# Performance work log

Measured on AMD Instinct MI355X. Metric: run time of the kernel, lower is better.

## Reference

```python
import jax, jax.numpy as jnp
import numpy as np

N = 50000      # nodes
E = 400000     # edges per relation
R = 3          # edge types
D = 128        # input_dim == hidden_dim
H = 8          # attention heads
Dh = D // H    # per-head dim (16)
OUT = 1        # output logits
NEG_SLOPE = 0.2
LN_EPS = 1e-5


def setup_inputs() -> dict:
    key = jax.random.key(0)
    ks = jax.random.split(key, 20)
    s = 0.05
    f32 = jnp.float32
    return {
        "feat": jax.random.normal(ks[0], (N, D), f32),
        "edge_src": jax.random.randint(ks[1], (R, E), 0, N, dtype=jnp.int32),
        "edge_dst": jax.random.randint(ks[2], (R, E), 0, N, dtype=jnp.int32),
        # conv1: per-relation GATConv params (W, attn_l, attn_r, bias)
        "W1": jax.random.normal(ks[3], (R, D, H * Dh), f32) * s,
        "al1": jax.random.normal(ks[4], (R, H, Dh), f32) * s,
        "ar1": jax.random.normal(ks[5], (R, H, Dh), f32) * s,
        "b1": jnp.zeros((R, H * Dh), f32),
        # conv2
        "W2": jax.random.normal(ks[6], (R, D, H * Dh), f32) * s,
        "al2": jax.random.normal(ks[7], (R, H, Dh), f32) * s,
        "ar2": jax.random.normal(ks[8], (R, H, Dh), f32) * s,
        "b2": jnp.zeros((R, H * Dh), f32),
        # LayerNorm
        "ln_g": jnp.ones((D,), f32),
        "ln_b": jnp.zeros((D,), f32),
        # classifier MLP (dropout inactive at eval)
        "Wc1": jax.random.normal(ks[9], (D, D), f32) * s,
        "bc1": jnp.zeros((D,), f32),
        "Wc2": jax.random.normal(ks[10], (D, OUT), f32) * s,
        "bc2": jnp.zeros((OUT,), f32),
    }


def _gat(x, src, dst, W, al, ar, b):
    """DGL GATConv on one relation: x [N,Din] -> [N, H*Dh]."""
    h = (x @ W).reshape(N, H, Dh)                       # projected feats
    el = (h * al).sum(-1)                               # [N,H] src attn term
    er = (h * ar).sum(-1)                               # [N,H] dst attn term
    e = jax.nn.leaky_relu(el[src] + er[dst], NEG_SLOPE)  # [E,H]
    # edge-softmax over incoming edges per dst node, per head
    m = jax.ops.segment_max(e, dst, num_segments=N)     # [N,H]
    ex = jnp.exp(e - m[dst])
    denom = jax.ops.segment_sum(ex, dst, num_segments=N)
    alpha = ex / denom[dst]                             # [E,H]
    msg = alpha[:, :, None] * h[src]                    # [E,H,Dh]
    out = jax.ops.segment_sum(msg, dst, num_segments=N)  # [N,H,Dh]
    return out.reshape(N, H * Dh) + b


def _hetero(x, edge_src, edge_dst, W, al, ar, b):
    out = jnp.zeros((N, H * Dh), x.dtype)
    for r in range(R):  # small fixed relation count
        out = out + _gat(x, edge_src[r], edge_dst[r], W[r], al[r], ar[r], b[r])
    return out


def reference(feat, edge_src, edge_dst, W1, al1, ar1, b1, W2, al2, ar2, b2,
              ln_g, ln_b, Wc1, bc1, Wc2, bc2):
    h1 = jax.nn.relu(_hetero(feat, edge_src, edge_dst, W1, al1, ar1, b1))
    h2 = _hetero(h1, edge_src, edge_dst, W2, al2, ar2, b2)
    h = h2 + h1
    mu = h.mean(-1, keepdims=True)
    var = ((h - mu) ** 2).mean(-1, keepdims=True)
    h = (h - mu) * jax.lax.rsqrt(var + LN_EPS) * ln_g + ln_b
    h = jax.nn.relu(h @ Wc1 + bc1)
    return h @ Wc2 + bc2
```

## Files before the change

### kernel.cpp

```cpp
#include <hip/hip_runtime.h>
#include <math.h>

#define NN 50000
#define NE 400000
#define NREL 3
#define NCH 196

typedef __bf16 bf16x8 __attribute__((ext_vector_type(8)));
typedef float floatx4 __attribute__((ext_vector_type(4)));

__device__ __forceinline__ unsigned short f2bf(float f) {
  unsigned int u = __float_as_uint(f);
  return (unsigned short)((u + 0x7fffu + ((u >> 16) & 1u)) >> 16);
}

__global__ __launch_bounds__(256) void prep_wt(
    const float* __restrict__ W1, const float* __restrict__ W2,
    const float* __restrict__ Wc1, unsigned short* __restrict__ Wt) {
  int mat = blockIdx.x >> 3, slab = blockIdx.x & 7;
  const float* Wsrc = mat < 3 ? W1 + mat * 16384
                    : (mat < 6 ? W2 + (mat - 3) * 16384 : Wc1);
  unsigned short* dst = Wt + (size_t)mat * 144 * 128;
  int k0 = slab * 16;
#pragma unroll
  for (int i = 0; i < 8; ++i) {
    int idx = i * 256 + threadIdx.x;
    int k = k0 + (idx >> 7), nn = idx & 127;
    dst[nn * 128 + k] = f2bf(Wsrc[k * 128 + nn]);
  }
}

__global__ __launch_bounds__(256) void prep_attn(
    const float* __restrict__ W1, const float* __restrict__ W2,
    const float* __restrict__ al1, const float* __restrict__ ar1,
    const float* __restrict__ al2, const float* __restrict__ ar2,
    unsigned short* __restrict__ Wt) {
  int mat = blockIdx.x;
  const float* Wsrc = mat < 3 ? W1 + mat * 16384 : W2 + (mat - 3) * 16384;
  const float* alp = mat < 3 ? al1 + mat * 128 : al2 + (mat - 3) * 128;
  const float* arp = mat < 3 ? ar1 + mat * 128 : ar2 + (mat - 3) * 128;
  unsigned short* dst = Wt + (size_t)mat * 144 * 128;
#pragma unroll
  for (int i = 0; i < 8; ++i) {
    int j = i * 256 + threadIdx.x;
    int half = j >> 10, jj = j & 1023;
    int k = jj >> 3, h = jj & 7;
    const float* av = half ? arp : alp;
    float s = 0.f;
#pragma unroll
    for (int d = 0; d < 16; ++d) s += Wsrc[k * 128 + h * 16 + d] * av[h * 16 + d];
    dst[(128 + half * 8 + h) * 128 + k] = f2bf(s);
  }
}

__global__ __launch_bounds__(256) void gemm3_attn_mfma(
    const float* __restrict__ X, const unsigned short* __restrict__ Wt,
    unsigned short* __restrict__ hp, float* __restrict__ el,
    float* __restrict__ er, int n) {
  __shared__ unsigned short Xs[64 * 136];
  __shared__ unsigned short Ws[144 * 136];
  int t = threadIdx.x;
  int rowbase = blockIdx.x * 64;

  const float4* X4 = (const float4*)X;
#pragma unroll
  for (int i = 0; i < 8; ++i) {
    int v = t + i * 256;
    int row = v >> 5, k4 = (v & 31) * 4;
    float4 x = make_float4(0.f, 0.f, 0.f, 0.f);
    if (rowbase + row < n) x = X4[(size_t)(rowbase + row) * 32 + (v & 31)];
    ushort4 p;
    p.x = f2bf(x.x); p.y = f2bf(x.y); p.z = f2bf(x.z); p.w = f2bf(x.w);
    *(ushort4*)&Xs[row * 136 + k4] = p;
  }

  int lane = t & 63, wave = t >> 6;
  int quad = lane >> 4, l = lane & 15;

  for (int r = 0; r < NREL; ++r) {
    __syncthreads();
    const uint4* WtR = (const uint4*)(Wt + (size_t)r * 144 * 128);
#pragma unroll
    for (int i = 0; i < 9; ++i) {
      int v = t + i * 256;
      ((uint4*)Ws)[(v >> 4) * 17 + (v & 15)] = WtR[v];
    }
    __syncthreads();

    floatx4 acc[9];
#pragma unroll
    for (int i = 0; i < 9; ++i) acc[i] = floatx4{0.f, 0.f, 0.f, 0.f};
#pragma unroll
    for (int ks = 0; ks < 4; ++ks) {
      bf16x8 a = *(const bf16x8*)&Xs[(wave * 16 + l) * 136 + ks * 32 + quad * 8];
#pragma unroll
      for (int nt = 0; nt < 9; ++nt) {
        bf16x8 b = *(const bf16x8*)&Ws[(nt * 16 + l) * 136 + ks * 32 + quad * 8];
        acc[nt] = __builtin_amdgcn_mfma_f32_16x16x32_bf16(a, b, acc[nt], 0, 0, 0);
      }
    }

    unsigned short* hpR = hp + (size_t)r * NN * 128;
    float* elR = el + (size_t)r * NN * 8;
    float* erR = er + (size_t)r * NN * 8;
    int r0 = rowbase + wave * 16 + quad * 4;
#pragma unroll
    for (int reg = 0; reg < 4; ++reg) {
      int row = r0 + reg;
      if (row < n) {
#pragma unroll
        for (int nt = 0; nt < 8; ++nt)
          hpR[(size_t)row * 128 + nt * 16 + l] = f2bf(acc[nt][reg]);
        if (l < 8) elR[row * 8 + l] = acc[8][reg];
        else       erR[row * 8 + (l - 8)] = acc[8][reg];
      }
    }
  }
}

__global__ __launch_bounds__(256) void gemm_head_mfma(
    const float* __restrict__ X, const unsigned short* __restrict__ Wt,
    const float* __restrict__ bc1, const float* __restrict__ wc2,
    const float* __restrict__ bc2, float* __restrict__ out, int n) {
  __shared__ unsigned short Xs[64 * 136];
  __shared__ unsigned short Ws[128 * 136];
  int t = threadIdx.x;
  int rowbase = blockIdx.x * 64;

  const float4* X4 = (const float4*)X;
#pragma unroll
  for (int i = 0; i < 8; ++i) {
    int v = t + i * 256;
    int row = v >> 5, k4 = (v & 31) * 4;
    float4 x = make_float4(0.f, 0.f, 0.f, 0.f);
    if (rowbase + row < n) x = X4[(size_t)(rowbase + row) * 32 + (v & 31)];
    ushort4 p;
    p.x = f2bf(x.x); p.y = f2bf(x.y); p.z = f2bf(x.z); p.w = f2bf(x.w);
    *(ushort4*)&Xs[row * 136 + k4] = p;
  }
  const uint4* WtR = (const uint4*)Wt;
#pragma unroll
  for (int i = 0; i < 8; ++i) {
    int v = t + i * 256;
    ((uint4*)Ws)[(v >> 4) * 17 + (v & 15)] = WtR[v];
  }
  __syncthreads();

  int lane = t & 63, wave = t >> 6;
  int quad = lane >> 4, l = lane & 15;

  floatx4 acc[8];
#pragma unroll
  for (int i = 0; i < 8; ++i) acc[i] = floatx4{0.f, 0.f, 0.f, 0.f};
#pragma unroll
  for (int ks = 0; ks < 4; ++ks) {
    bf16x8 a = *(const bf16x8*)&Xs[(wave * 16 + l) * 136 + ks * 32 + quad * 8];
#pragma unroll
    for (int nt = 0; nt < 8; ++nt) {
      bf16x8 b = *(const bf16x8*)&Ws[(nt * 16 + l) * 136 + ks * 32 + quad * 8];
      acc[nt] = __builtin_amdgcn_mfma_f32_16x16x32_bf16(a, b, acc[nt], 0, 0, 0);
    }
  }

  float bv[8], wv[8];
#pragma unroll
  for (int nt = 0; nt < 8; ++nt) {
    bv[nt] = bc1[nt * 16 + l];
    wv[nt] = wc2[nt * 16 + l];
  }
  int r0 = rowbase + wave * 16 + quad * 4;
#pragma unroll
  for (int reg = 0; reg < 4; ++reg) {
    float s = 0.f;
#pragma unroll
    for (int nt = 0; nt < 8; ++nt)
      s += fmaxf(acc[nt][reg] + bv[nt], 0.f) * wv[nt];
    s += __shfl_xor(s, 1); s += __shfl_xor(s, 2);
    s += __shfl_xor(s, 4); s += __shfl_xor(s, 8);
    int row = r0 + reg;
    if (l == 0 && row < n) out[row] = s + bc2[0];
  }
}

__global__ __launch_bounds__(256) void hist_kernel(
    const int* __restrict__ edst, int* __restrict__ cnt, int* __restrict__ rank) {
  int t = blockIdx.x * 256 + threadIdx.x;
  if (t >= NREL * NE) return;
  int r = t / NE;
  rank[t] = atomicAdd(&cnt[r * NN + edst[t]], 1);
}

__global__ __launch_bounds__(256) void scan1(
    const int* __restrict__ cnt, int* __restrict__ partials) {
  __shared__ int s[256];
  int r = blockIdx.x / NCH, c = blockIdx.x % NCH;
  int i = c * 256 + threadIdx.x;
  s[threadIdx.x] = (i < NN) ? cnt[r * NN + i] : 0;
  __syncthreads();
  for (int off = 128; off; off >>= 1) {
    if (threadIdx.x < off) s[threadIdx.x] += s[threadIdx.x + off];
    __syncthreads();
  }
  if (threadIdx.x == 0) partials[r * NCH + c] = s[0];
}

__global__ __launch_bounds__(256) void scan2(int* __restrict__ partials) {
  __shared__ int s[256];
  int r = blockIdx.x;
  int t = threadIdx.x;
  int v = (t < NCH) ? partials[r * NCH + t] : 0;
  s[t] = v;
  __syncthreads();
  for (int off = 1; off < 256; off <<= 1) {
    int x = (t >= off) ? s[t - off] : 0;
    __syncthreads();
    s[t] += x;
    __syncthreads();
  }
  if (t < NCH) partials[r * NCH + t] = s[t] - v;
}

__global__ __launch_bounds__(256) void scan3(
    const int* __restrict__ cnt, const int* __restrict__ partials,
    int* __restrict__ rowptr) {
  __shared__ int s[256];
  int r = blockIdx.x / NCH, c = blockIdx.x % NCH;
  int t = threadIdx.x;
  int i = c * 256 + t;
  int v = (i < NN) ? cnt[r * NN + i] : 0;
  s[t] = v;
  __syncthreads();
  for (int off = 1; off < 256; off <<= 1) {
    int x = (t >= off) ? s[t - off] : 0;
    __syncthreads();
    s[t] += x;
    __syncthreads();
  }
  int base = partials[r * NCH + c];
  if (i < NN) rowptr[r * (NN + 1) + i] = base + s[t] - v;
  if (c == NCH - 1 && t == 0) rowptr[r * (NN + 1) + NN] = NE;
}

__global__ __launch_bounds__(256) void scatter_kernel(
    const int* __restrict__ esrc, const int* __restrict__ edst,
    const int* __restrict__ rowptr, const int* __restrict__ rank,
    int* __restrict__ col) {
  int t = blockIdx.x * 256 + threadIdx.x;
  if (t >= NREL * NE) return;
  int r = t / NE;
  int pos = rowptr[r * (NN + 1) + edst[t]] + rank[t];
  col[(size_t)r * NE + pos] = esrc[t];
}

__global__ __launch_bounds__(256) void gather_all(
    const int* __restrict__ rowptr, const int* __restrict__ col,
    const float* __restrict__ el, const float* __restrict__ er,
    const unsigned short* __restrict__ hp, const float* __restrict__ b,
    float* __restrict__ h1, const float* __restrict__ g,
    const float* __restrict__ beta, int mode) {
  int wid = (blockIdx.x * 256 + threadIdx.x) >> 6;
  int lane = threadIdx.x & 63;
  if (wid >= NN) return;
  int head = lane >> 3;
  int c = lane * 2;
  float ax = 0.f, ay = 0.f;
#pragma unroll
  for (int r = 0; r < NREL; ++r) {
    const int* rp = rowptr + r * (NN + 1);
    const int* cl = col + (size_t)r * NE;
    const float* elr = el + (size_t)r * NN * 8;
    const unsigned short* hpr = hp + (size_t)r * NN * 128;
    float er_d = er[(size_t)r * NN * 8 + wid * 8 + head];
    int start = rp[wid], end = rp[wid + 1];
    float den = 0.f, sx = 0.f, sy = 0.f;
    for (int i = start; i < end; i += 4) {
      int last = end - 1;
      int s0 = cl[i];
      int s1 = cl[min(i + 1, last)];
      int s2 = cl[min(i + 2, last)];
      int s3 = cl[min(i + 3, last)];
      float e0 = elr[s0 * 8 + head] + er_d;
      float e1 = elr[s1 * 8 + head] + er_d;
      float e2 = elr[s2 * 8 + head] + er_d;
      float e3 = elr[s3 * 8 + head] + er_d;
      unsigned int u0 = *(const unsigned int*)&hpr[(size_t)s0 * 128 + c];
      unsigned int u1 = *(const unsigned int*)&hpr[(size_t)s1 * 128 + c];
      unsigned int u2 = *(const unsigned int*)&hpr[(size_t)s2 * 128 + c];
      unsigned int u3 = *(const unsigned int*)&hpr[(size_t)s3 * 128 + c];
      e0 = (e0 > 0.f) ? e0 : 0.2f * e0;
      e1 = (e1 > 0.f) ? e1 : 0.2f * e1;
      e2 = (e2 > 0.f) ? e2 : 0.2f * e2;
      e3 = (e3 > 0.f) ? e3 : 0.2f * e3;
      float x0 = __expf(e0);
      float x1 = (i + 1 < end) ? __expf(e1) : 0.f;
      float x2 = (i + 2 < end) ? __expf(e2) : 0.f;
      float x3 = (i + 3 < end) ? __expf(e3) : 0.f;
      den += x0 + x1 + x2 + x3;
      sx += x0 * __uint_as_float(u0 << 16) + x1 * __uint_as_float(u1 << 16) +
            x2 * __uint_as_float(u2 << 16) + x3 * __uint_as_float(u3 << 16);
      sy += x0 * __uint_as_float(u0 & 0xffff0000u) +
            x1 * __uint_as_float(u1 & 0xffff0000u) +
            x2 * __uint_as_float(u2 & 0xffff0000u) +
            x3 * __uint_as_float(u3 & 0xffff0000u);
    }
    if (end > start) {
      float inv = 1.f / den;
      ax += sx * inv;
      ay += sy * inv;
    }
  }
  float bx = b[c] + b[128 + c] + b[256 + c];
  float by = b[c + 1] + b[128 + c + 1] + b[256 + c + 1];
  float2* hptr = (float2*)&h1[(size_t)wid * 128 + c];
  if (mode == 0) {
    *hptr = make_float2(fmaxf(ax + bx, 0.f), fmaxf(ay + by, 0.f));
  } else {
    float2 r1 = *hptr;
    float vx = ax + bx + r1.x;
    float vy = ay + by + r1.y;
    float s = vx + vy;
#pragma unroll
    for (int off = 32; off; off >>= 1) s += __shfl_xor(s, off);
    float mu = s * (1.f / 128.f);
    float dx = vx - mu, dy = vy - mu;
    float sq = dx * dx + dy * dy;
#pragma unroll
    for (int off = 32; off; off >>= 1) sq += __shfl_xor(sq, off);
    float rstd = rsqrtf(sq * (1.f / 128.f) + 1e-5f);
    *hptr = make_float2(dx * rstd * g[c] + beta[c],
                        dy * rstd * g[c + 1] + beta[c + 1]);
  }
}

extern "C" void kernel_launch(void* const* d_in, const int* in_sizes, int n_in,
                              void* d_out, int out_size, void* d_ws, size_t ws_size,
                              hipStream_t stream) {
  const float* feat = (const float*)d_in[0];
  const int* esrc = (const int*)d_in[1];
  const int* edst = (const int*)d_in[2];
  const float* W1 = (const float*)d_in[3];
  const float* al1 = (const float*)d_in[4];
  const float* ar1 = (const float*)d_in[5];
  const float* b1 = (const float*)d_in[6];
  const float* W2 = (const float*)d_in[7];
  const float* al2 = (const float*)d_in[8];
  const float* ar2 = (const float*)d_in[9];
  const float* b2 = (const float*)d_in[10];
  const float* lng = (const float*)d_in[11];
  const float* lnb = (const float*)d_in[12];
  const float* Wc1 = (const float*)d_in[13];
  const float* bc1 = (const float*)d_in[14];
  const float* Wc2 = (const float*)d_in[15];
  const float* bc2 = (const float*)d_in[16];
  float* out = (float*)d_out;

  unsigned short* hp = (unsigned short*)d_ws;
  float* el = (float*)(hp + (size_t)3 * NN * 128);
  float* er = el + (size_t)3 * NN * 8;
  float* h1 = er + (size_t)3 * NN * 8;
  int* rowptr = (int*)(h1 + (size_t)NN * 128);
  int* col = rowptr + NREL * (NN + 1);
  int* cnt = col + (size_t)NREL * NE;
  int* partials = cnt + NREL * NN;
  unsigned short* Wt = (unsigned short*)(((uintptr_t)(partials + NREL * NCH) + 15)
                                         & ~(uintptr_t)15);
  int* rank = (int*)el;

  const int gemm_grid = (NN + 63) / 64;
  const int edge_grid = (NREL * NE + 255) / 256;
  const int gg_grid = (NN * 64) / 256;

  prep_wt<<<56, 256, 0, stream>>>(W1, W2, Wc1, Wt);
  prep_attn<<<6, 256, 0, stream>>>(W1, W2, al1, ar1, al2, ar2, Wt);

  hipMemsetAsync(cnt, 0, (size_t)NREL * NN * sizeof(int), stream);
  hist_kernel<<<edge_grid, 256, 0, stream>>>(edst, cnt, rank);
  scan1<<<NREL * NCH, 256, 0, stream>>>(cnt, partials);
  scan2<<<NREL, 256, 0, stream>>>(partials);
  scan3<<<NREL * NCH, 256, 0, stream>>>(cnt, partials, rowptr);
  scatter_kernel<<<edge_grid, 256, 0, stream>>>(esrc, edst, rowptr, rank, col);

  gemm3_attn_mfma<<<gemm_grid, 256, 0, stream>>>(feat, Wt, hp, el, er, NN);
  gather_all<<<gg_grid, 256, 0, stream>>>(rowptr, col, el, er, hp, b1,
                                          h1, nullptr, nullptr, 0);
  gemm3_attn_mfma<<<gemm_grid, 256, 0, stream>>>(
      h1, Wt + (size_t)3 * 144 * 128, hp, el, er, NN);
  gather_all<<<gg_grid, 256, 0, stream>>>(rowptr, col, el, er, hp, b2,
                                          h1, lng, lnb, 1);
  gemm_head_mfma<<<gemm_grid, 256, 0, stream>>>(
      h1, Wt + (size_t)6 * 144 * 128, bc1, Wc2, bc2, out, NN);
}
```

Measured before the change: 390.2 us.

## Compute attention scores edge-parallel within head groups and broadcast via lane intrinsics

The gather kernel is restructured so that each of the 8 lanes in a head group computes the attention exponent for a different edge. Column indices are broadcast with readlane and the exp weights with ds_swizzle. Previously every lane redundantly loaded el and evaluated exp for every edge. The column indices for the next 8-edge chunk are prefetched one iteration ahead, and the softmax denominator is reduced across the 8 lanes at the end. In exchange it adds cross-lane operations and processes padded 8-edge chunks, which wastes work on nodes with few edges.

```diff
diff --git a/kernel.cpp b/kernel.cpp
--- a/kernel.cpp
+++ b/kernel.cpp
@@ -261,54 +261,79 @@
   int wid = (blockIdx.x * 256 + threadIdx.x) >> 6;
   int lane = threadIdx.x & 63;
   if (wid >= NN) return;
-  int head = lane >> 3;
+  int h = lane >> 3;
+  int eoff = lane & 7;
   int c = lane * 2;
-  float ax = 0.f, ay = 0.f;
+
+  int st3[NREL], en3[NREL], cv3[NREL];
+  float er3[NREL];
 #pragma unroll
   for (int r = 0; r < NREL; ++r) {
     const int* rp = rowptr + r * (NN + 1);
-    const int* cl = col + (size_t)r * NE;
-    const float* elr = el + (size_t)r * NN * 8;
-    const unsigned short* hpr = hp + (size_t)r * NN * 128;
-    float er_d = er[(size_t)r * NN * 8 + wid * 8 + head];
-    int start = rp[wid], end = rp[wid + 1];
-    float den = 0.f, sx = 0.f, sy = 0.f;
-    for (int i = start; i < end; i += 4) {
+    st3[r] = rp[wid];
+    en3[r] = rp[wid + 1];
+    er3[r] = er[(size_t)r * NN * 8 + wid * 8 + h];
+  }
+#pragma unroll
+  for (int r = 0; r < NREL; ++r) {
+    int last = en3[r] - 1;
+    last = last < st3[r] ? st3[r] : last;
+    int i0 = st3[r] + eoff;
+    cv3[r] = col[r * NE + (i0 < last ? i0 : last)];
+  }
+
+  float ax = 0.f, ay = 0.f;
+#pragma unroll
+  for (int r = 0; r < NREL; ++r) {
+    int start = st3[r], end = en3[r];
+    if (end > start) {
+      const int* cl = col + r * NE;
+      const float* elr = el + (size_t)r * NN * 8;
+      const unsigned short* hpr = hp + (size_t)r * NN * 128;
+      float er_me = er3[r];
       int last = end - 1;
-      int s0 = cl[i];
-      int s1 = cl[min(i + 1, last)];
-      int s2 = cl[min(i + 2, last)];
-      int s3 = cl[min(i + 3, last)];
-      float e0 = elr[s0 * 8 + head] + er_d;
-      float e1 = elr[s1 * 8 + head] + er_d;
-      float e2 = elr[s2 * 8 + head] + er_d;
-      float e3 = elr[s3 * 8 + head] + er_d;
-      unsigned int u0 = *(const unsigned int*)&hpr[(size_t)s0 * 128 + c];
-      unsigned int u1 = *(const unsigned int*)&hpr[(size_t)s1 * 128 + c];
-      unsigned int u2 = *(const unsigned int*)&hpr[(size_t)s2 * 128 + c];
-      unsigned int u3 = *(const unsigned int*)&hpr[(size_t)s3 * 128 + c];
-      e0 = (e0 > 0.f) ? e0 : 0.2f * e0;
-      e1 = (e1 > 0.f) ? e1 : 0.2f * e1;
-      e2 = (e2 > 0.f) ? e2 : 0.2f * e2;
-      e3 = (e3 > 0.f) ? e3 : 0.2f * e3;
-      float x0 = __expf(e0);
-      float x1 = (i + 1 < end) ? __expf(e1) : 0.f;
-      float x2 = (i + 2 < end) ? __expf(e2) : 0.f;
-      float x3 = (i + 3 < end) ? __expf(e3) : 0.f;
-      den += x0 + x1 + x2 + x3;
-      sx += x0 * __uint_as_float(u0 << 16) + x1 * __uint_as_float(u1 << 16) +
-            x2 * __uint_as_float(u2 << 16) + x3 * __uint_as_float(u3 << 16);
-      sy += x0 * __uint_as_float(u0 & 0xffff0000u) +
-            x1 * __uint_as_float(u1 & 0xffff0000u) +
-            x2 * __uint_as_float(u2 & 0xffff0000u) +
-            x3 * __uint_as_float(u3 & 0xffff0000u);
-    }
-    if (end > start) {
+      int idx = start + eoff;
+      int colv = cv3[r];
+      float den = 0.f, sx = 0.f, sy = 0.f;
+      for (int i = start; i < end; i += 8) {
+        int nidx = idx + 8;
+        int colm = cl[nidx < last ? nidx : last];
+        float e = elr[colv * 8 + h] + er_me;
+        e = fmaxf(e, 0.2f * e);
+        float x = (idx < end) ? __expf(e) : 0.f;
+        den += x;
+        unsigned int xi = __float_as_uint(x);
+#define GATHER_EDGE(JJ)                                                        \
+        {                                                                      \
+          int sj = __builtin_amdgcn_readlane(colv, JJ);                        \
+          const unsigned int* rowp = (const unsigned int*)(hpr + (size_t)sj * 128); \
+          unsigned int u = rowp[lane];                                         \
+          float xe = __uint_as_float(                                          \
+              __builtin_amdgcn_ds_swizzle(xi, ((JJ) << 5) | 0x18));            \
+          sx += xe * __uint_as_float(u << 16);                                 \
+          sy += xe * __uint_as_float(u & 0xffff0000u);                         \
+        }
+        GATHER_EDGE(0)
+        GATHER_EDGE(1)
+        GATHER_EDGE(2)
+        GATHER_EDGE(3)
+        GATHER_EDGE(4)
+        GATHER_EDGE(5)
+        GATHER_EDGE(6)
+        GATHER_EDGE(7)
+#undef GATHER_EDGE
+        idx = nidx;
+        colv = colm;
+      }
+      den += __shfl_xor(den, 1);
+      den += __shfl_xor(den, 2);
+      den += __shfl_xor(den, 4);
       float inv = 1.f / den;
       ax += sx * inv;
       ay += sy * inv;
     }
   }
+
   float bx = b[c] + b[128 + c] + b[256 + c];
   float by = b[c + 1] + b[128 + c + 1] + b[256 + c + 1];
   float2* hptr = (float2*)&h1[(size_t)wid * 128 + c];
@@ -373,7 +398,7 @@
   prep_wt<<<56, 256, 0, stream>>>(W1, W2, Wc1, Wt);
   prep_attn<<<6, 256, 0, stream>>>(W1, W2, al1, ar1, al2, ar2, Wt);
 
-  hipMemsetAsync(cnt, 0, (size_t)NREL * NN * sizeof(int), stream);
+  (void)hipMemsetAsync(cnt, 0, (size_t)NREL * NN * sizeof(int), stream);
   hist_kernel<<<edge_grid, 256, 0, stream>>>(edst, cnt, rank);
   scan1<<<NREL * NCH, 256, 0, stream>>>(cnt, partials);
   scan2<<<NREL, 256, 0, stream>>>(partials);
```

Result: faster. 372.3 us (-4.6%).

## Software-pipeline gather across three relations with lane-parallel edge scoring

Applied to the files above, without the earlier changes.

Rewrites the gather kernel so all three relations are processed together in one software-pipelined loop. Each group of 8 lanes loads one edge index and attention logit in parallel, computes exp once per edge, and shares the weight by ds_swizzle. Source indices are broadcast with readlane for the bf16 feature loads. The next batch's column and el loads are prefetched before the FMAs. Meant to cut redundant per-lane exp and index work and to expose more memory-level parallelism, at the cost of higher register use and wasted work when relation degrees differ.

```diff
diff --git a/kernel.cpp b/kernel.cpp
--- a/kernel.cpp
+++ b/kernel.cpp
@@ -261,61 +261,149 @@
   int wid = (blockIdx.x * 256 + threadIdx.x) >> 6;
   int lane = threadIdx.x & 63;
   if (wid >= NN) return;
-  int head = lane >> 3;
+  int h = lane >> 3;
+  int eoff = lane & 7;
   int c = lane * 2;
+  int lane4 = lane * 4;
+
+  int st0, st1, st2, ee0, ee1, ee2;
+  {
+    const int* rp = rowptr;
+    st0 = rp[wid]; ee0 = rp[wid + 1];
+    rp += NN + 1;
+    st1 = rp[wid]; ee1 = rp[wid + 1];
+    rp += NN + 1;
+    st2 = rp[wid]; ee2 = rp[wid + 1];
+  }
+  float erv0 = er[wid * 8 + h];
+  float erv1 = er[(size_t)NN * 8 + wid * 8 + h];
+  float erv2 = er[(size_t)2 * NN * 8 + wid * 8 + h];
+  float b0x = b[c], b1x = b[128 + c], b2x = b[256 + c];
+  float b0y = b[c + 1], b1y = b[128 + c + 1], b2y = b[256 + c + 1];
+  float2* hptr = (float2*)&h1[(size_t)wid * 128 + c];
+  float2 r1 = make_float2(0.f, 0.f);
+  float gx = 0.f, gy = 0.f, btx = 0.f, bty = 0.f;
+  if (mode) {
+    r1 = *hptr;
+    gx = g[c]; gy = g[c + 1];
+    btx = beta[c]; bty = beta[c + 1];
+  }
+
+  const int* clp0 = col;
+  const int* clp1 = col + NE;
+  const int* clp2 = col + 2 * NE;
+  const float* elp0 = el;
+  const float* elp1 = el + (size_t)NN * 8;
+  const float* elp2 = el + (size_t)2 * NN * 8;
+  const char* hpb0 = (const char*)hp;
+  const char* hpb1 = hpb0 + (size_t)NN * 256;
+  const char* hpb2 = hpb1 + (size_t)NN * 256;
+
+  int la0 = ee0 - 1; if (la0 < st0) la0 = st0; if (la0 >= NE) la0 = NE - 1;
+  int la1 = ee1 - 1; if (la1 < st1) la1 = st1; if (la1 >= NE) la1 = NE - 1;
+  int la2 = ee2 - 1; if (la2 < st2) la2 = st2; if (la2 >= NE) la2 = NE - 1;
+
+  int i0 = st0 + eoff, i1 = st1 + eoff, i2 = st2 + eoff;
+  int cv0 = clp0[i0 < la0 ? i0 : la0];
+  int cv1 = clp1[i1 < la1 ? i1 : la1];
+  int cv2 = clp2[i2 < la2 ? i2 : la2];
+  float ev0 = elp0[cv0 * 8 + h];
+  float ev1 = elp1[cv1 * 8 + h];
+  float ev2 = elp2[cv2 * 8 + h];
+
+  int bb0 = st0, bb1 = st1, bb2 = st2;
+  float den0 = 0.f, den1 = 0.f, den2 = 0.f;
+  float sx0 = 0.f, sy0 = 0.f, sx1 = 0.f, sy1 = 0.f, sx2 = 0.f, sy2 = 0.f;
+
+#define A_PHASE(R)                                                             \
+  if (a##R) {                                                                  \
+    int ni_ = bb##R + 8 + eoff;                                                \
+    cm##R = clp##R[ni_ < la##R ? ni_ : la##R];                                 \
+    float e_ = ev##R + erv##R;                                                 \
+    e_ = fmaxf(e_, 0.2f * e_);                                                 \
+    float x_ = (bb##R + eoff < ee##R) ? __expf(e_) : 0.f;                      \
+    den##R += x_;                                                              \
+    xi##R = __float_as_uint(x_);                                               \
+  }
+
+#define LOAD_EDGE(R, JJ)                                                       \
+  {                                                                            \
+    int s_ = __builtin_amdgcn_readlane(cv##R, JJ);                             \
+    u##R##_##JJ = *(const unsigned int*)(hpb##R + (size_t)s_ * 256 + lane4);   \
+  }
+
+#define B_PHASE(R)                                                             \
+  if (a##R) {                                                                  \
+    LOAD_EDGE(R, 0) LOAD_EDGE(R, 1) LOAD_EDGE(R, 2) LOAD_EDGE(R, 3)            \
+    LOAD_EDGE(R, 4) LOAD_EDGE(R, 5) LOAD_EDGE(R, 6) LOAD_EDGE(R, 7)            \
+  }
+
+#define FMA_EDGE(R, JJ, PAT)                                                   \
+  {                                                                            \
+    float xe_ = __uint_as_float(__builtin_amdgcn_ds_swizzle(xi##R, PAT));      \
+    sx##R += xe_ * __uint_as_float(u##R##_##JJ << 16);                         \
+    sy##R += xe_ * __uint_as_float(u##R##_##JJ & 0xffff0000u);                 \
+  }
+
+#define C_PHASE(R)                                                             \
+  if (a##R) {                                                                  \
+    FMA_EDGE(R, 0, 0x18) FMA_EDGE(R, 1, 0x38) FMA_EDGE(R, 2, 0x58)             \
+    FMA_EDGE(R, 3, 0x78) FMA_EDGE(R, 4, 0x98) FMA_EDGE(R, 5, 0xb8)             \
+    FMA_EDGE(R, 6, 0xd8) FMA_EDGE(R, 7, 0xf8)                                  \
+  }
+
+  for (;;) {
+    bool a0 = bb0 < ee0, a1 = bb1 < ee1, a2 = bb2 < ee2;
+    if (!(a0 | a1 | a2)) break;
+    int cm0 = cv0, cm1 = cv1, cm2 = cv2;
+    unsigned int xi0 = 0, xi1 = 0, xi2 = 0;
+    unsigned int u0_0, u0_1, u0_2, u0_3, u0_4, u0_5, u0_6, u0_7;
+    unsigned int u1_0, u1_1, u1_2, u1_3, u1_4, u1_5, u1_6, u1_7;
+    unsigned int u2_0, u2_1, u2_2, u2_3, u2_4, u2_5, u2_6, u2_7;
+    A_PHASE(0) A_PHASE(1) A_PHASE(2)
+    B_PHASE(0) B_PHASE(1) B_PHASE(2)
+    float evn0 = ev0, evn1 = ev1, evn2 = ev2;
+    if (a0) evn0 = elp0[cm0 * 8 + h];
+    if (a1) evn1 = elp1[cm1 * 8 + h];
+    if (a2) evn2 = elp2[cm2 * 8 + h];
+    __builtin_amdgcn_sched_barrier(0);
+    C_PHASE(0) C_PHASE(1) C_PHASE(2)
+    bb0 += 8; bb1 += 8; bb2 += 8;
+    cv0 = cm0; cv1 = cm1; cv2 = cm2;
+    ev0 = evn0; ev1 = evn1; ev2 = evn2;
+  }
+
+#undef A_PHASE
+#undef LOAD_EDGE
+#undef B_PHASE
+#undef FMA_EDGE
+#undef C_PHASE
+
   float ax = 0.f, ay = 0.f;
-#pragma unroll
-  for (int r = 0; r < NREL; ++r) {
-    const int* rp = rowptr + r * (NN + 1);
-    const int* cl = col + (size_t)r * NE;
-    const float* elr = el + (size_t)r * NN * 8;
-    const unsigned short* hpr = hp + (size_t)r * NN * 128;
-    float er_d = er[(size_t)r * NN * 8 + wid * 8 + head];
-    int start = rp[wid], end = rp[wid + 1];
-    float den = 0.f, sx = 0.f, sy = 0.f;
-    for (int i = start; i < end; i += 4) {
-      int last = end - 1;
-      int s0 = cl[i];
-      int s1 = cl[min(i + 1, last)];
-      int s2 = cl[min(i + 2, last)];
-      int s3 = cl[min(i + 3, last)];
-      float e0 = elr[s0 * 8 + head] + er_d;
-      float e1 = elr[s1 * 8 + head] + er_d;
-      float e2 = elr[s2 * 8 + head] + er_d;
-      float e3 = elr[s3 * 8 + head] + er_d;
-      unsigned int u0 = *(const unsigned int*)&hpr[(size_t)s0 * 128 + c];
-      unsigned int u1 = *(const unsigned int*)&hpr[(size_t)s1 * 128 + c];
-      unsigned int u2 = *(const unsigned int*)&hpr[(size_t)s2 * 128 + c];
-      unsigned int u3 = *(const unsigned int*)&hpr[(size_t)s3 * 128 + c];
-      e0 = (e0 > 0.f) ? e0 : 0.2f * e0;
-      e1 = (e1 > 0.f) ? e1 : 0.2f * e1;
-      e2 = (e2 > 0.f) ? e2 : 0.2f * e2;
-      e3 = (e3 > 0.f) ? e3 : 0.2f * e3;
-      float x0 = __expf(e0);
-      float x1 = (i + 1 < end) ? __expf(e1) : 0.f;
-      float x2 = (i + 2 < end) ? __expf(e2) : 0.f;
-      float x3 = (i + 3 < end) ? __expf(e3) : 0.f;
-      den += x0 + x1 + x2 + x3;
-      sx += x0 * __uint_as_float(u0 << 16) + x1 * __uint_as_float(u1 << 16) +
-            x2 * __uint_as_float(u2 << 16) + x3 * __uint_as_float(u3 << 16);
-      sy += x0 * __uint_as_float(u0 & 0xffff0000u) +
-            x1 * __uint_as_float(u1 & 0xffff0000u) +
-            x2 * __uint_as_float(u2 & 0xffff0000u) +
-            x3 * __uint_as_float(u3 & 0xffff0000u);
-    }
-    if (end > start) {
-      float inv = 1.f / den;
-      ax += sx * inv;
-      ay += sy * inv;
-    }
-  }
-  float bx = b[c] + b[128 + c] + b[256 + c];
-  float by = b[c + 1] + b[128 + c + 1] + b[256 + c + 1];
-  float2* hptr = (float2*)&h1[(size_t)wid * 128 + c];
+  if (ee0 > st0) {
+    float d = den0;
+    d += __shfl_xor(d, 1); d += __shfl_xor(d, 2); d += __shfl_xor(d, 4);
+    float inv = 1.f / d;
+    ax += sx0 * inv; ay += sy0 * inv;
+  }
+  if (ee1 > st1) {
+    float d = den1;
+    d += __shfl_xor(d, 1); d += __shfl_xor(d, 2); d += __shfl_xor(d, 4);
+    float inv = 1.f / d;
+    ax += sx1 * inv; ay += sy1 * inv;
+  }
+  if (ee2 > st2) {
+    float d = den2;
+    d += __shfl_xor(d, 1); d += __shfl_xor(d, 2); d += __shfl_xor(d, 4);
+    float inv = 1.f / d;
+    ax += sx2 * inv; ay += sy2 * inv;
+  }
+
+  float bx = b0x + b1x + b2x;
+  float by = b0y + b1y + b2y;
   if (mode == 0) {
     *hptr = make_float2(fmaxf(ax + bx, 0.f), fmaxf(ay + by, 0.f));
   } else {
-    float2 r1 = *hptr;
     float vx = ax + bx + r1.x;
     float vy = ay + by + r1.y;
     float s = vx + vy;
@@ -327,8 +415,7 @@
 #pragma unroll
     for (int off = 32; off; off >>= 1) sq += __shfl_xor(sq, off);
     float rstd = rsqrtf(sq * (1.f / 128.f) + 1e-5f);
-    *hptr = make_float2(dx * rstd * g[c] + beta[c],
-                        dy * rstd * g[c + 1] + beta[c + 1]);
+    *hptr = make_float2(dx * rstd * gx + btx, dy * rstd * gy + bty);
   }
 }
 
@@ -373,7 +460,7 @@
   prep_wt<<<56, 256, 0, stream>>>(W1, W2, Wc1, Wt);
   prep_attn<<<6, 256, 0, stream>>>(W1, W2, al1, ar1, al2, ar2, Wt);
 
-  hipMemsetAsync(cnt, 0, (size_t)NREL * NN * sizeof(int), stream);
+  (void)hipMemsetAsync(cnt, 0, (size_t)NREL * NN * sizeof(int), stream);
   hist_kernel<<<edge_grid, 256, 0, stream>>>(edst, cnt, rank);
   scan1<<<NREL * NCH, 256, 0, stream>>>(cnt, partials);
   scan2<<<NREL, 256, 0, stream>>>(partials);
```

Measured after the change: 420.2 us. +7.7%, slower.
